# Kernel tuning notes

Hardware: AMD Instinct MI355X
Metric: run time of the kernel (lower is better)

The kernel has to match this reference:

```python
import jax, jax.numpy as jnp
import numpy as np

DIM = 256
BUFFER_SIZE = 64


def setup_inputs() -> dict:
    key = jax.random.key(0)
    k1, k2, k3 = jax.random.split(key, 3)
    B, S, D = 4, 4096, DIM
    d2 = 2 * D
    states = jax.random.normal(k1, (B, S, D, 2), dtype=jnp.float32)
    # nn.Linear weights, applied as x @ W.T (torch convention)
    W_q = jax.random.normal(k2, (d2, d2), dtype=jnp.float32) / np.sqrt(d2)
    W_k = jax.random.normal(k3, (d2, d2), dtype=jnp.float32) / np.sqrt(d2)
    return {"states": states, "W_q": W_q, "W_k": W_k}


def reference(states, W_q, W_k):
    B, S, D, _ = states.shape
    d2 = 2 * D
    states_flat = states.reshape(B, S, d2)                      # [B,S,2D]
    queries = jnp.einsum('bsd,ed->bse', states_flat, W_q)       # x @ W.T
    keys = jnp.einsum('bsd,ed->bse', states_flat, W_k)
    scale = d2 ** -0.5
    scores = jnp.einsum('bqe,bke->bqk', queries, keys) * scale  # [B,S,S]
    pos = jnp.arange(S)
    diff = pos[:, None] - pos[None, :]                          # i - j
    # causal (strictly past) AND within sliding window of buffer_size
    valid = (diff >= 1) & (diff <= BUFFER_SIZE)                 # [S,S]
    scores = jnp.where(valid[None, :, :], scores, -jnp.inf)
    attn = jax.nn.softmax(scores, axis=-1)
    attn = jnp.nan_to_num(attn, nan=0.0)                        # row 0 is all -inf -> 0
    retrieved = jnp.einsum('bqk,bkd->bqd', attn, states_flat)   # values = raw states
    return retrieved.reshape(B, S, D, 2), attn
```

## Files before the change

kernel.cpp:

```cpp
#include <hip/hip_runtime.h>
#include <hip/hip_bf16.h>
#include <cstdint>

typedef uint16_t u16;
typedef __attribute__((ext_vector_type(8))) short short8;
typedef __attribute__((ext_vector_type(4))) float f32x4;
typedef __attribute__((ext_vector_type(2))) float f32x2;
typedef __attribute__((ext_vector_type(4))) float fv4;

static constexpr int S = 4096;
static constexpr int D2 = 512;
static constexpr size_t RET_ELEMS = 16384ull * 512ull;
static constexpr float SCALE = 0.04419417382415922f;

__device__ __forceinline__ u16 f2bf(float f) {
  uint32_t u = __float_as_uint(f);
  u += 0x7fffu + ((u >> 16) & 1u);
  return (u16)(u >> 16);
}

__device__ __forceinline__ float bflo(uint32_t u) { return __uint_as_float(u << 16); }
__device__ __forceinline__ float bfhi(uint32_t u) { return __uint_as_float(u & 0xffff0000u); }

__global__ void cast_f32_bf16(const float* __restrict__ src, u16* __restrict__ dst, int n4) {
  int idx = blockIdx.x * blockDim.x + threadIdx.x;
  if (idx < n4) {
    float4 v = *(const float4*)(src + (size_t)idx * 4);
    ushort4 o;
    o.x = f2bf(v.x); o.y = f2bf(v.y); o.z = f2bf(v.z); o.w = f2bf(v.w);
    *(ushort4*)(dst + (size_t)idx * 4) = o;
  }
}

#define BM 128
#define BN 128
#define BK 32
#define LDSP 40

__global__ __launch_bounds__(256) void qk_gemm(
    const u16* __restrict__ Xb, const u16* __restrict__ Wqb, const u16* __restrict__ Wkb,
    u16* __restrict__ Qb, u16* __restrict__ Kb) {
  __shared__ u16 Xs[BM * LDSP];
  __shared__ u16 Ws[BN * LDSP];
  const int m0 = blockIdx.x * BM;
  const int sel = blockIdx.y >> 2;
  const int n0 = (blockIdx.y & 3) * BN;
  const u16* __restrict__ Wb = sel ? Wkb : Wqb;
  u16* __restrict__ Cb = sel ? Kb : Qb;

  const int t = threadIdx.x;
  const int lane = t & 63, w = t >> 6;
  const int wm = w >> 1, wn = w & 1;
  const int r16 = lane & 15, kg = lane >> 4;
  const int srow = t >> 2, skcol = (t & 3) * 8;

  f32x4 acc[4][4] = {};

  for (int kt = 0; kt < D2; kt += BK) {
    __syncthreads();
    for (int p = 0; p < 2; ++p) {
      int row = srow + p * 64;
      uint4 va = *(const uint4*)(Xb + (size_t)(m0 + row) * D2 + kt + skcol);
      *(uint4*)(Xs + row * LDSP + skcol) = va;
      uint4 vb = *(const uint4*)(Wb + (size_t)(n0 + row) * D2 + kt + skcol);
      *(uint4*)(Ws + row * LDSP + skcol) = vb;
    }
    __syncthreads();
    short8 a[4], b[4];
    for (int f = 0; f < 4; ++f) {
      a[f] = *(const short8*)(Xs + (wm * 64 + f * 16 + r16) * LDSP + kg * 8);
      b[f] = *(const short8*)(Ws + (wn * 64 + f * 16 + r16) * LDSP + kg * 8);
    }
    for (int fm = 0; fm < 4; ++fm)
      for (int fn = 0; fn < 4; ++fn)
        acc[fm][fn] = __builtin_amdgcn_mfma_f32_16x16x32_bf16(a[fm], b[fn], acc[fm][fn], 0, 0, 0);
  }

  for (int fm = 0; fm < 4; ++fm) {
    int grow = m0 + wm * 64 + fm * 16 + kg * 4;
    for (int fn = 0; fn < 4; ++fn) {
      int gcol = n0 + wn * 64 + fn * 16 + r16;
      for (int r = 0; r < 4; ++r)
        Cb[(size_t)(grow + r) * D2 + gcol] = f2bf(acc[fm][fn][r]);
    }
  }
}

__global__ __launch_bounds__(256, 4) void attn_kernel(
    const u16* __restrict__ Qb, const u16* __restrict__ Kb, const u16* __restrict__ Xb,
    float* __restrict__ out) {
  __shared__ float p_jm[4][80][16];

  const int bid = blockIdx.x;
  const int swz = (bid & 7) * 128 + (bid >> 3);
  const int w = threadIdx.x >> 6;
  const int lane = threadIdx.x & 63;
  const int qg = swz * 16;
  const int b = qg >> 12;
  const int i0 = qg & (S - 1);
  const int c15 = lane & 15;
  const int g = lane >> 4;

  const u16* kbat = Kb + (((size_t)b) << 12) * D2;
  const u16* qptr = Qb + (size_t)(qg + c15) * D2 + g * 8;
  const u16* kptr = kbat + (ptrdiff_t)(i0 - 64 + c15) * D2 + g * 8;
  float* azero = out + RET_ELEMS + (size_t)qg * S;

  f32x4 sc[5] = {};
  const fv4 z4 = {0.f, 0.f, 0.f, 0.f};
  #pragma unroll 1
  for (int s = 0; s < 16; ++s) {
    short8 qf = *(const short8*)(qptr + s * 32);
    #pragma unroll
    for (int r_ = 0; r_ < 4; ++r_) {
      const int rw = 4 * w + r_;
      const int i = i0 + rw;
      const int f = s * 64 + lane;
      const int flo = (i >= 64) ? ((i - 64) >> 2) : 0;
      const bool band = (i >= 1) && (f >= flo) && (f <= ((i - 1) >> 2));
      if (!band)
        __builtin_nontemporal_store(z4, (fv4*)(azero + (size_t)rw * S + 4 * f));
    }
    #pragma unroll
    for (int t = 0; t < 5; ++t) {
      short8 kf = *(const short8*)(kptr + t * (16 * D2) + s * 32);
      sc[t] = __builtin_amdgcn_mfma_f32_16x16x32_bf16(qf, kf, sc[t], 0, 0, 0);
    }
  }

  float sv[5][4];
  #pragma unroll
  for (int t = 0; t < 5; ++t)
    #pragma unroll
    for (int r = 0; r < 4; ++r) {
      const int m = 4 * g + r;
      const int rel = 16 * t + c15 - m;
      const int j = i0 - 64 + 16 * t + c15;
      const bool ok = (rel >= 0) && (rel < 64) && (j >= 0);
      sv[t][r] = ok ? sc[t][r] * SCALE : -INFINITY;
    }

  float p[5][4];
  #pragma unroll
  for (int r = 0; r < 4; ++r) {
    float mx = sv[0][r];
    #pragma unroll
    for (int t = 1; t < 5; ++t) mx = fmaxf(mx, sv[t][r]);
    #pragma unroll
    for (int off = 8; off; off >>= 1) mx = fmaxf(mx, __shfl_xor(mx, off));
    float e[5], sum = 0.f;
    #pragma unroll
    for (int t = 0; t < 5; ++t) {
      e[t] = (sv[t][r] == -INFINITY) ? 0.f : __expf(sv[t][r] - mx);
      sum += e[t];
    }
    #pragma unroll
    for (int off = 8; off; off >>= 1) sum += __shfl_xor(sum, off);
    const float rinv = (sum > 0.f) ? 1.f / sum : 0.f;
    #pragma unroll
    for (int t = 0; t < 5; ++t) p[t][r] = e[t] * rinv;
  }

  #pragma unroll
  for (int t = 0; t < 5; ++t)
    #pragma unroll
    for (int r = 0; r < 4; ++r)
      p_jm[w][16 * t + c15][4 * g + r] = p[t][r];

  {
    const int m2 = 4 * w + g;
    const int i = i0 + m2;
    if (i >= 1) {
      const int lo = (i >= 64) ? (i - 64) : 0;
      const int f0 = lo >> 2, f1 = (i - 1) >> 2;
      float* arow = azero + (size_t)m2 * S;
      #pragma unroll
      for (int pass = 0; pass < 2; ++pass) {
        const int f = f0 + c15 + 16 * pass;
        if (f <= f1) {
          fv4 v;
          #pragma unroll
          for (int c = 0; c < 4; ++c) {
            const int col = 4 * f + c;
            const bool in = (col >= lo) && (col <= i - 1);
            v[c] = in ? p_jm[w][col - i0 + 64][m2] : 0.f;
          }
          __builtin_nontemporal_store(v, (fv4*)(arow + 4 * f));
        }
      }
    }
  }

  f32x2 acc[16];
  #pragma unroll
  for (int m = 0; m < 16; ++m) acc[m] = (f32x2){0.f, 0.f};

  const int jstart = (i0 >= 64) ? 0 : (64 - i0);
  const u16* xcol = Xb + (((size_t)b) << 12) * D2 + (ptrdiff_t)(i0 - 64) * D2
                    + w * 128 + lane * 2;
  #pragma unroll 2
  for (int j = jstart; j < 79; ++j) {
    const uint32_t xu = *(const uint32_t*)(xcol + (size_t)j * D2);
    const f32x2 xv = {bflo(xu), bfhi(xu)};
    float pall[16];
    *(float4*)&pall[0]  = *(const float4*)&p_jm[w][j][0];
    *(float4*)&pall[4]  = *(const float4*)&p_jm[w][j][4];
    *(float4*)&pall[8]  = *(const float4*)&p_jm[w][j][8];
    *(float4*)&pall[12] = *(const float4*)&p_jm[w][j][12];
    #pragma unroll
    for (int m = 0; m < 16; ++m)
      acc[m] += (f32x2){pall[m], pall[m]} * xv;
  }

  #pragma unroll
  for (int m = 0; m < 16; ++m) {
    float* rr = out + (size_t)(qg + m) * D2 + w * 128 + lane * 2;
    __builtin_nontemporal_store(acc[m], (f32x2*)rr);
  }
}

extern "C" void kernel_launch(void* const* d_in, const int* in_sizes, int n_in,
                              void* d_out, int out_size, void* d_ws, size_t ws_size,
                              hipStream_t stream) {
  const float* states = (const float*)d_in[0];
  const float* W_q    = (const float*)d_in[1];
  const float* W_k    = (const float*)d_in[2];
  float* out = (float*)d_out;

  char* ws = (char*)d_ws;
  u16* Xb  = (u16*)(ws);
  u16* Qb  = (u16*)(ws + 16777216);
  u16* Kb  = (u16*)(ws + 33554432);
  u16* Wqb = (u16*)(ws + 50331648);
  u16* Wkb = (u16*)(ws + 50855936);

  cast_f32_bf16<<<8192, 256, 0, stream>>>(states, Xb, 2097152);
  cast_f32_bf16<<<256, 256, 0, stream>>>(W_q, Wqb, 65536);
  cast_f32_bf16<<<256, 256, 0, stream>>>(W_k, Wkb, 65536);

  qk_gemm<<<dim3(128, 8), 256, 0, stream>>>(Xb, Wqb, Wkb, Qb, Kb);

  attn_kernel<<<1024, 256, 0, stream>>>(Qb, Kb, Xb, out);
}
```

Baseline: 128.3 us.

## Fold Wq^T Wk into one matrix and compute scores against states in LDS

New measurement: 145.6 us. 13.5% more time.

```diff
diff --git a/kernel.cpp b/kernel.cpp
--- a/kernel.cpp
+++ b/kernel.cpp
@@ -5,7 +5,6 @@
 typedef uint16_t u16;
 typedef __attribute__((ext_vector_type(8))) short short8;
 typedef __attribute__((ext_vector_type(4))) float f32x4;
-typedef __attribute__((ext_vector_type(2))) float f32x2;
 typedef __attribute__((ext_vector_type(4))) float fv4;
 
 static constexpr int S = 4096;
@@ -32,21 +31,46 @@
   }
 }
 
+__global__ __launch_bounds__(256) void m_gemm(const float* __restrict__ Wq,
+                                              const float* __restrict__ Wk,
+                                              u16* __restrict__ MbT) {
+  __shared__ float aq[8][32], ak[8][32];
+  const int d0 = (blockIdx.x & 15) * 32;
+  const int e0 = (blockIdx.x >> 4) * 32;
+  const int tx = threadIdx.x & 15, ty = threadIdx.x >> 4;
+  float acc[2][2] = {};
+  for (int k0 = 0; k0 < 512; k0 += 8) {
+    __syncthreads();
+    const int r = threadIdx.x >> 5, c = threadIdx.x & 31;
+    aq[r][c] = Wq[(size_t)(k0 + r) * 512 + d0 + c];
+    ak[r][c] = Wk[(size_t)(k0 + r) * 512 + e0 + c];
+    __syncthreads();
+    #pragma unroll
+    for (int kk = 0; kk < 8; ++kk) {
+      const float q0 = aq[kk][2 * ty], q1 = aq[kk][2 * ty + 1];
+      const float w0 = ak[kk][2 * tx], w1 = ak[kk][2 * tx + 1];
+      acc[0][0] += q0 * w0; acc[0][1] += q0 * w1;
+      acc[1][0] += q1 * w0; acc[1][1] += q1 * w1;
+    }
+  }
+  #pragma unroll
+  for (int a = 0; a < 2; ++a)
+    #pragma unroll
+    for (int c = 0; c < 2; ++c)
+      MbT[(size_t)(e0 + 2 * tx + c) * 512 + d0 + 2 * ty + a] = f2bf(acc[a][c] * SCALE);
+}
+
 #define BM 128
 #define BN 128
 #define BK 32
 #define LDSP 40
 
-__global__ __launch_bounds__(256) void qk_gemm(
-    const u16* __restrict__ Xb, const u16* __restrict__ Wqb, const u16* __restrict__ Wkb,
-    u16* __restrict__ Qb, u16* __restrict__ Kb) {
+__global__ __launch_bounds__(256) void q_gemm(
+    const u16* __restrict__ Xb, const u16* __restrict__ Bt, u16* __restrict__ Qp) {
   __shared__ u16 Xs[BM * LDSP];
   __shared__ u16 Ws[BN * LDSP];
   const int m0 = blockIdx.x * BM;
-  const int sel = blockIdx.y >> 2;
-  const int n0 = (blockIdx.y & 3) * BN;
-  const u16* __restrict__ Wb = sel ? Wkb : Wqb;
-  u16* __restrict__ Cb = sel ? Kb : Qb;
+  const int n0 = blockIdx.y * BN;
 
   const int t = threadIdx.x;
   const int lane = t & 63, w = t >> 6;
@@ -62,7 +86,7 @@
       int row = srow + p * 64;
       uint4 va = *(const uint4*)(Xb + (size_t)(m0 + row) * D2 + kt + skcol);
       *(uint4*)(Xs + row * LDSP + skcol) = va;
-      uint4 vb = *(const uint4*)(Wb + (size_t)(n0 + row) * D2 + kt + skcol);
+      uint4 vb = *(const uint4*)(Bt + (size_t)(n0 + row) * D2 + kt + skcol);
       *(uint4*)(Ws + row * LDSP + skcol) = vb;
     }
     __syncthreads();
@@ -81,109 +105,138 @@
     for (int fn = 0; fn < 4; ++fn) {
       int gcol = n0 + wn * 64 + fn * 16 + r16;
       for (int r = 0; r < 4; ++r)
-        Cb[(size_t)(grow + r) * D2 + gcol] = f2bf(acc[fm][fn][r]);
-    }
-  }
-}
-
-__global__ __launch_bounds__(256, 4) void attn_kernel(
-    const u16* __restrict__ Qb, const u16* __restrict__ Kb, const u16* __restrict__ Xb,
-    float* __restrict__ out) {
+        Qp[(size_t)(grow + r) * D2 + gcol] = f2bf(acc[fm][fn][r]);
+    }
+  }
+}
+
+__global__ __launch_bounds__(512) void attn_kernel(
+    const u16* __restrict__ Qp, const u16* __restrict__ Xb, float* __restrict__ out) {
+  __shared__ u16 xs[128 * 512];
   __shared__ float p_jm[4][80][16];
 
   const int bid = blockIdx.x;
-  const int swz = (bid & 7) * 128 + (bid >> 3);
+  const int swz = (bid & 7) * 32 + (bid >> 3);
   const int w = threadIdx.x >> 6;
   const int lane = threadIdx.x & 63;
-  const int qg = swz * 16;
+  const int qg = swz * 64;
   const int b = qg >> 12;
   const int i0 = qg & (S - 1);
-  const int c15 = lane & 15;
-  const int g = lane >> 4;
-
-  const u16* kbat = Kb + (((size_t)b) << 12) * D2;
-  const u16* qptr = Qb + (size_t)(qg + c15) * D2 + g * 8;
-  const u16* kptr = kbat + (ptrdiff_t)(i0 - 64 + c15) * D2 + g * 8;
-  float* azero = out + RET_ELEMS + (size_t)qg * S;
-
-  f32x4 sc[5] = {};
+  const int c15 = lane & 15, g = lane >> 4;
+  const int grp = w & 3, dh = w >> 2;
+  const int i0g = i0 + grp * 16;
+  const int qgg = qg + grp * 16;
+
+  float* aout = out + RET_ELEMS + (size_t)qg * S;
   const fv4 z4 = {0.f, 0.f, 0.f, 0.f};
-  #pragma unroll 1
-  for (int s = 0; s < 16; ++s) {
-    short8 qf = *(const short8*)(qptr + s * 32);
-    #pragma unroll
-    for (int r_ = 0; r_ < 4; ++r_) {
-      const int rw = 4 * w + r_;
-      const int i = i0 + rw;
-      const int f = s * 64 + lane;
+
+  {
+    const u16* xbat = Xb + (((size_t)b) << 12) * D2;
+    const int tid = threadIdx.x;
+    #pragma unroll
+    for (int cch = 0; cch < 16; ++cch) {
+      const int idx8 = tid + (cch << 9);
+      const int rl = idx8 >> 6;
+      const int cb = (idx8 & 63) << 4;
+      int gr = i0 - 64 + rl; gr = gr < 0 ? 0 : gr;
+      const uint4 v = *(const uint4*)(xbat + (size_t)gr * D2 + (cb >> 1));
+      *(uint4*)((char*)xs + rl * 1024 + (cb ^ ((rl & 7) << 4))) = v;
+    }
+  }
+  __syncthreads();
+
+  if (dh == 0) {
+    const u16* qptr = Qp + (size_t)(qgg + c15) * D2 + g * 8;
+    f32x4 sc[5] = {};
+    #pragma unroll 1
+    for (int s = 0; s < 16; ++s) {
+      const short8 qf = *(const short8*)(qptr + s * 32);
+      #pragma unroll
+      for (int t = 0; t < 5; ++t) {
+        const int rl = grp * 16 + 16 * t + c15;
+        const int cb = ((s << 6) + (g << 4)) ^ ((rl & 7) << 4);
+        const short8 kf = *(const short8*)((const char*)xs + rl * 1024 + cb);
+        sc[t] = __builtin_amdgcn_mfma_f32_16x16x32_bf16(qf, kf, sc[t], 0, 0, 0);
+      }
+    }
+
+    float sv[5][4];
+    #pragma unroll
+    for (int t = 0; t < 5; ++t)
+      #pragma unroll
+      for (int r = 0; r < 4; ++r) {
+        const int m = 4 * g + r;
+        const int rel = 16 * t + c15 - m;
+        const int j = i0g - 64 + 16 * t + c15;
+        const bool ok = (rel >= 0) && (rel < 64) && (j >= 0);
+        sv[t][r] = ok ? sc[t][r] : -INFINITY;
+      }
+
+    float p[5][4];
+    #pragma unroll
+    for (int r = 0; r < 4; ++r) {
+      float mx = sv[0][r];
+      #pragma unroll
+      for (int t = 1; t < 5; ++t) mx = fmaxf(mx, sv[t][r]);
+      #pragma unroll
+      for (int off = 8; off; off >>= 1) mx = fmaxf(mx, __shfl_xor(mx, off));
+      float e[5], sum = 0.f;
+      #pragma unroll
+      for (int t = 0; t < 5; ++t) {
+        e[t] = (sv[t][r] == -INFINITY) ? 0.f : __expf(sv[t][r] - mx);
+        sum += e[t];
+      }
+      #pragma unroll
+      for (int off = 8; off; off >>= 1) sum += __shfl_xor(sum, off);
+      const float rinv = (sum > 0.f) ? 1.f / sum : 0.f;
+      #pragma unroll
+      for (int t = 0; t < 5; ++t) p[t][r] = e[t] * rinv;
+    }
+
+    #pragma unroll
+    for (int t = 0; t < 5; ++t)
+      #pragma unroll
+      for (int r = 0; r < 4; ++r)
+        p_jm[grp][16 * t + c15][4 * g + r] = p[t][r];
+  } else {
+    #pragma unroll 1
+    for (int rr = 0; rr < 16; ++rr) {
+      const int m2 = grp * 16 + rr;
+      const int i = i0 + m2;
       const int flo = (i >= 64) ? ((i - 64) >> 2) : 0;
-      const bool band = (i >= 1) && (f >= flo) && (f <= ((i - 1) >> 2));
-      if (!band)
-        __builtin_nontemporal_store(z4, (fv4*)(azero + (size_t)rw * S + 4 * f));
-    }
-    #pragma unroll
-    for (int t = 0; t < 5; ++t) {
-      short8 kf = *(const short8*)(kptr + t * (16 * D2) + s * 32);
-      sc[t] = __builtin_amdgcn_mfma_f32_16x16x32_bf16(qf, kf, sc[t], 0, 0, 0);
-    }
-  }
-
-  float sv[5][4];
-  #pragma unroll
-  for (int t = 0; t < 5; ++t)
-    #pragma unroll
-    for (int r = 0; r < 4; ++r) {
-      const int m = 4 * g + r;
-      const int rel = 16 * t + c15 - m;
-      const int j = i0 - 64 + 16 * t + c15;
-      const bool ok = (rel >= 0) && (rel < 64) && (j >= 0);
-      sv[t][r] = ok ? sc[t][r] * SCALE : -INFINITY;
-    }
-
-  float p[5][4];
-  #pragma unroll
-  for (int r = 0; r < 4; ++r) {
-    float mx = sv[0][r];
-    #pragma unroll
-    for (int t = 1; t < 5; ++t) mx = fmaxf(mx, sv[t][r]);
-    #pragma unroll
-    for (int off = 8; off; off >>= 1) mx = fmaxf(mx, __shfl_xor(mx, off));
-    float e[5], sum = 0.f;
-    #pragma unroll
-    for (int t = 0; t < 5; ++t) {
-      e[t] = (sv[t][r] == -INFINITY) ? 0.f : __expf(sv[t][r] - mx);
-      sum += e[t];
-    }
-    #pragma unroll
-    for (int off = 8; off; off >>= 1) sum += __shfl_xor(sum, off);
-    const float rinv = (sum > 0.f) ? 1.f / sum : 0.f;
-    #pragma unroll
-    for (int t = 0; t < 5; ++t) p[t][r] = e[t] * rinv;
-  }
-
-  #pragma unroll
-  for (int t = 0; t < 5; ++t)
-    #pragma unroll
-    for (int r = 0; r < 4; ++r)
-      p_jm[w][16 * t + c15][4 * g + r] = p[t][r];
+      const int f1b = (i - 1) >> 2;
+      float* arow = aout + (size_t)m2 * S;
+      #pragma unroll 4
+      for (int s = 0; s < 16; ++s) {
+        const int f = s * 64 + lane;
+        const bool band = (i >= 1) && (f >= flo) && (f <= f1b);
+        if (!band) __builtin_nontemporal_store(z4, (fv4*)(arow + 4 * f));
+      }
+    }
+  }
+  __syncthreads();
 
   {
-    const int m2 = 4 * w + g;
+    const int mm = dh * 8 + g * 2 + (c15 >> 3);
+    const int m2 = grp * 16 + mm;
     const int i = i0 + m2;
+    const int c8 = c15 & 7;
     if (i >= 1) {
       const int lo = (i >= 64) ? (i - 64) : 0;
       const int f0 = lo >> 2, f1 = (i - 1) >> 2;
-      float* arow = azero + (size_t)m2 * S;
-      #pragma unroll
-      for (int pass = 0; pass < 2; ++pass) {
-        const int f = f0 + c15 + 16 * pass;
+      float* arow = aout + (size_t)m2 * S;
+      #pragma unroll
+      for (int pass = 0; pass < 3; ++pass) {
+        const int f = f0 + c8 + (pass << 3);
         if (f <= f1) {
           fv4 v;
           #pragma unroll
           for (int c = 0; c < 4; ++c) {
             const int col = 4 * f + c;
-            const bool in = (col >= lo) && (col <= i - 1);
-            v[c] = in ? p_jm[w][col - i0 + 64][m2] : 0.f;
+            const bool in = (col >= lo) && (col < i);
+            int rel = col - (i0g - 64);
+            rel = rel < 0 ? 0 : rel;
+            v[c] = in ? p_jm[grp][rel][mm] : 0.f;
           }
           __builtin_nontemporal_store(v, (fv4*)(arow + 4 * f));
         }
@@ -191,31 +244,34 @@
     }
   }
 
-  f32x2 acc[16];
-  #pragma unroll
-  for (int m = 0; m < 16; ++m) acc[m] = (f32x2){0.f, 0.f};
-
-  const int jstart = (i0 >= 64) ? 0 : (64 - i0);
-  const u16* xcol = Xb + (((size_t)b) << 12) * D2 + (ptrdiff_t)(i0 - 64) * D2
-                    + w * 128 + lane * 2;
+  f32x4 acc[16] = {};
+  const int jstart = (i0g >= 64) ? 0 : (64 - i0g);
+  const int cbase = (dh << 9) + (lane << 3);
   #pragma unroll 2
   for (int j = jstart; j < 79; ++j) {
-    const uint32_t xu = *(const uint32_t*)(xcol + (size_t)j * D2);
-    const f32x2 xv = {bflo(xu), bfhi(xu)};
-    float pall[16];
-    *(float4*)&pall[0]  = *(const float4*)&p_jm[w][j][0];
-    *(float4*)&pall[4]  = *(const float4*)&p_jm[w][j][4];
-    *(float4*)&pall[8]  = *(const float4*)&p_jm[w][j][8];
-    *(float4*)&pall[12] = *(const float4*)&p_jm[w][j][12];
-    #pragma unroll
-    for (int m = 0; m < 16; ++m)
-      acc[m] += (f32x2){pall[m], pall[m]} * xv;
-  }
-
-  #pragma unroll
+    const int rl = grp * 16 + j;
+    const int cb = cbase ^ ((rl & 7) << 4);
+    const uint2 xu = *(const uint2*)((const char*)xs + rl * 1024 + cb);
+    const float x0 = bflo(xu.x), x1 = bfhi(xu.x);
+    const float x2 = bflo(xu.y), x3 = bfhi(xu.y);
+    alignas(16) float pall[16];
+    *(float4*)&pall[0]  = *(const float4*)&p_jm[grp][j][0];
+    *(float4*)&pall[4]  = *(const float4*)&p_jm[grp][j][4];
+    *(float4*)&pall[8]  = *(const float4*)&p_jm[grp][j][8];
+    *(float4*)&pall[12] = *(const float4*)&p_jm[grp][j][12];
+    #pragma unroll
+    for (int m = 0; m < 16; ++m) {
+      const fv4 xv = {x0, x1, x2, x3};
+      const fv4 pp = {pall[m], pall[m], pall[m], pall[m]};
+      acc[m] += pp * xv;
+    }
+  }
+
+  #pragma unroll 1
   for (int m = 0; m < 16; ++m) {
-    float* rr = out + (size_t)(qg + m) * D2 + w * 128 + lane * 2;
-    __builtin_nontemporal_store(acc[m], (f32x2*)rr);
+    float* rr = out + (size_t)(qgg + m) * D2 + (dh << 8) + lane * 4;
+    const fv4 r = {acc[m][0], acc[m][1], acc[m][2], acc[m][3]};
+    __builtin_nontemporal_store(r, (fv4*)rr);
   }
 }
 
@@ -229,16 +285,11 @@
 
   char* ws = (char*)d_ws;
   u16* Xb  = (u16*)(ws);
-  u16* Qb  = (u16*)(ws + 16777216);
-  u16* Kb  = (u16*)(ws + 33554432);
-  u16* Wqb = (u16*)(ws + 50331648);
-  u16* Wkb = (u16*)(ws + 50855936);
+  u16* Qp  = (u16*)(ws + 16777216);
+  u16* MbT = (u16*)(ws + 33554432);
 
   cast_f32_bf16<<<8192, 256, 0, stream>>>(states, Xb, 2097152);
-  cast_f32_bf16<<<256, 256, 0, stream>>>(W_q, Wqb, 65536);
-  cast_f32_bf16<<<256, 256, 0, stream>>>(W_k, Wkb, 65536);
-
-  qk_gemm<<<dim3(128, 8), 256, 0, stream>>>(Xb, Wqb, Wkb, Qb, Kb);
-
-  attn_kernel<<<1024, 256, 0, stream>>>(Qb, Kb, Xb, out);
-}
+  m_gemm<<<256, 256, 0, stream>>>(W_q, W_k, MbT);
+  q_gemm<<<dim3(128, 4), 256, 0, stream>>>(Xb, MbT, Qp);
+  attn_kernel<<<256, 512, 0, stream>>>(Qp, Xb, out);
+}
```

## Fold Wq^T·Wk into one matrix and replace the separate K projection

Applied to the files above, without the earlier changes.

Result: slower. 184.1 us (+43.4%).

```diff
diff --git a/kernel.cpp b/kernel.cpp
--- a/kernel.cpp
+++ b/kernel.cpp
@@ -32,21 +32,46 @@
   }
 }
 
+__global__ __launch_bounds__(256) void m_gemm(const float* __restrict__ Wq,
+                                              const float* __restrict__ Wk,
+                                              u16* __restrict__ MbT) {
+  __shared__ float aq[8][32], ak[8][32];
+  const int d0 = (blockIdx.x & 15) * 32;
+  const int e0 = (blockIdx.x >> 4) * 32;
+  const int tx = threadIdx.x & 15, ty = threadIdx.x >> 4;
+  float acc[2][2] = {};
+  for (int k0 = 0; k0 < 512; k0 += 8) {
+    __syncthreads();
+    const int r = threadIdx.x >> 5, c = threadIdx.x & 31;
+    aq[r][c] = Wq[(size_t)(k0 + r) * 512 + d0 + c];
+    ak[r][c] = Wk[(size_t)(k0 + r) * 512 + e0 + c];
+    __syncthreads();
+    #pragma unroll
+    for (int kk = 0; kk < 8; ++kk) {
+      const float q0 = aq[kk][2 * ty], q1 = aq[kk][2 * ty + 1];
+      const float w0 = ak[kk][2 * tx], w1 = ak[kk][2 * tx + 1];
+      acc[0][0] += q0 * w0; acc[0][1] += q0 * w1;
+      acc[1][0] += q1 * w0; acc[1][1] += q1 * w1;
+    }
+  }
+  #pragma unroll
+  for (int a = 0; a < 2; ++a)
+    #pragma unroll
+    for (int c = 0; c < 2; ++c)
+      MbT[(size_t)(e0 + 2 * tx + c) * 512 + d0 + 2 * ty + a] = f2bf(acc[a][c] * SCALE);
+}
+
 #define BM 128
 #define BN 128
 #define BK 32
 #define LDSP 40
 
-__global__ __launch_bounds__(256) void qk_gemm(
-    const u16* __restrict__ Xb, const u16* __restrict__ Wqb, const u16* __restrict__ Wkb,
-    u16* __restrict__ Qb, u16* __restrict__ Kb) {
+__global__ __launch_bounds__(256) void q_gemm(
+    const u16* __restrict__ Xb, const u16* __restrict__ Bt, u16* __restrict__ Qp) {
   __shared__ u16 Xs[BM * LDSP];
   __shared__ u16 Ws[BN * LDSP];
   const int m0 = blockIdx.x * BM;
-  const int sel = blockIdx.y >> 2;
-  const int n0 = (blockIdx.y & 3) * BN;
-  const u16* __restrict__ Wb = sel ? Wkb : Wqb;
-  u16* __restrict__ Cb = sel ? Kb : Qb;
+  const int n0 = blockIdx.y * BN;
 
   const int t = threadIdx.x;
   const int lane = t & 63, w = t >> 6;
@@ -62,7 +87,7 @@
       int row = srow + p * 64;
       uint4 va = *(const uint4*)(Xb + (size_t)(m0 + row) * D2 + kt + skcol);
       *(uint4*)(Xs + row * LDSP + skcol) = va;
-      uint4 vb = *(const uint4*)(Wb + (size_t)(n0 + row) * D2 + kt + skcol);
+      uint4 vb = *(const uint4*)(Bt + (size_t)(n0 + row) * D2 + kt + skcol);
       *(uint4*)(Ws + row * LDSP + skcol) = vb;
     }
     __syncthreads();
@@ -81,14 +106,13 @@
     for (int fn = 0; fn < 4; ++fn) {
       int gcol = n0 + wn * 64 + fn * 16 + r16;
       for (int r = 0; r < 4; ++r)
-        Cb[(size_t)(grow + r) * D2 + gcol] = f2bf(acc[fm][fn][r]);
+        Qp[(size_t)(grow + r) * D2 + gcol] = f2bf(acc[fm][fn][r]);
     }
   }
 }
 
 __global__ __launch_bounds__(256, 4) void attn_kernel(
-    const u16* __restrict__ Qb, const u16* __restrict__ Kb, const u16* __restrict__ Xb,
-    float* __restrict__ out) {
+    const u16* __restrict__ Qp, const u16* __restrict__ Xb, float* __restrict__ out) {
   __shared__ float p_jm[4][80][16];
 
   const int bid = blockIdx.x;
@@ -98,32 +122,19 @@
   const int qg = swz * 16;
   const int b = qg >> 12;
   const int i0 = qg & (S - 1);
-  const int c15 = lane & 15;
-  const int g = lane >> 4;
-
-  const u16* kbat = Kb + (((size_t)b) << 12) * D2;
-  const u16* qptr = Qb + (size_t)(qg + c15) * D2 + g * 8;
-  const u16* kptr = kbat + (ptrdiff_t)(i0 - 64 + c15) * D2 + g * 8;
-  float* azero = out + RET_ELEMS + (size_t)qg * S;
+  const int c15 = lane & 15, g = lane >> 4;
+
+  const u16* xbat = Xb + (((size_t)b) << 12) * D2;
+  const u16* qptr = Qp + (size_t)(qg + c15) * D2 + g * 8;
+  const u16* kptr = xbat + (ptrdiff_t)(i0 - 64 + c15) * D2 + g * 8;
 
   f32x4 sc[5] = {};
-  const fv4 z4 = {0.f, 0.f, 0.f, 0.f};
   #pragma unroll 1
   for (int s = 0; s < 16; ++s) {
-    short8 qf = *(const short8*)(qptr + s * 32);
-    #pragma unroll
-    for (int r_ = 0; r_ < 4; ++r_) {
-      const int rw = 4 * w + r_;
-      const int i = i0 + rw;
-      const int f = s * 64 + lane;
-      const int flo = (i >= 64) ? ((i - 64) >> 2) : 0;
-      const bool band = (i >= 1) && (f >= flo) && (f <= ((i - 1) >> 2));
-      if (!band)
-        __builtin_nontemporal_store(z4, (fv4*)(azero + (size_t)rw * S + 4 * f));
-    }
+    const short8 qf = *(const short8*)(qptr + s * 32);
     #pragma unroll
     for (int t = 0; t < 5; ++t) {
-      short8 kf = *(const short8*)(kptr + t * (16 * D2) + s * 32);
+      const short8 kf = *(const short8*)(kptr + t * (16 * D2) + s * 32);
       sc[t] = __builtin_amdgcn_mfma_f32_16x16x32_bf16(qf, kf, sc[t], 0, 0, 0);
     }
   }
@@ -137,7 +148,7 @@
       const int rel = 16 * t + c15 - m;
       const int j = i0 - 64 + 16 * t + c15;
       const bool ok = (rel >= 0) && (rel < 64) && (j >= 0);
-      sv[t][r] = ok ? sc[t][r] * SCALE : -INFINITY;
+      sv[t][r] = ok ? sc[t][r] : -INFINITY;
     }
 
   float p[5][4];
@@ -173,7 +184,7 @@
     if (i >= 1) {
       const int lo = (i >= 64) ? (i - 64) : 0;
       const int f0 = lo >> 2, f1 = (i - 1) >> 2;
-      float* arow = azero + (size_t)m2 * S;
+      float* arow = out + RET_ELEMS + (size_t)(qg + m2) * S;
       #pragma unroll
       for (int pass = 0; pass < 2; ++pass) {
         const int f = f0 + c15 + 16 * pass;
@@ -182,8 +193,10 @@
           #pragma unroll
           for (int c = 0; c < 4; ++c) {
             const int col = 4 * f + c;
-            const bool in = (col >= lo) && (col <= i - 1);
-            v[c] = in ? p_jm[w][col - i0 + 64][m2] : 0.f;
+            const bool in = (col >= lo) && (col < i);
+            int rel = col - i0 + 64;
+            rel = (rel < 0) ? 0 : (rel > 79 ? 79 : rel);
+            v[c] = in ? p_jm[w][rel][m2] : 0.f;
           }
           __builtin_nontemporal_store(v, (fv4*)(arow + 4 * f));
         }
@@ -196,13 +209,12 @@
   for (int m = 0; m < 16; ++m) acc[m] = (f32x2){0.f, 0.f};
 
   const int jstart = (i0 >= 64) ? 0 : (64 - i0);
-  const u16* xcol = Xb + (((size_t)b) << 12) * D2 + (ptrdiff_t)(i0 - 64) * D2
-                    + w * 128 + lane * 2;
+  const u16* xcol = xbat + (ptrdiff_t)(i0 - 64) * D2 + w * 128 + lane * 2;
   #pragma unroll 2
   for (int j = jstart; j < 79; ++j) {
     const uint32_t xu = *(const uint32_t*)(xcol + (size_t)j * D2);
     const f32x2 xv = {bflo(xu), bfhi(xu)};
-    float pall[16];
+    alignas(16) float pall[16];
     *(float4*)&pall[0]  = *(const float4*)&p_jm[w][j][0];
     *(float4*)&pall[4]  = *(const float4*)&p_jm[w][j][4];
     *(float4*)&pall[8]  = *(const float4*)&p_jm[w][j][8];
@@ -228,17 +240,14 @@
   float* out = (float*)d_out;
 
   char* ws = (char*)d_ws;
-  u16* Xb  = (u16*)(ws);
-  u16* Qb  = (u16*)(ws + 16777216);
-  u16* Kb  = (u16*)(ws + 33554432);
-  u16* Wqb = (u16*)(ws + 50331648);
-  u16* Wkb = (u16*)(ws + 50855936);
+  u16* Qp  = (u16*)(ws);
+  u16* Xb  = (u16*)(ws + 16777216);
+  u16* MbT = (u16*)(ws + 33554432);
+
+  hipMemsetAsync(out + RET_ELEMS, 0, 16384ull * 4096ull * 4ull, stream);
 
   cast_f32_bf16<<<8192, 256, 0, stream>>>(states, Xb, 2097152);
-  cast_f32_bf16<<<256, 256, 0, stream>>>(W_q, Wqb, 65536);
-  cast_f32_bf16<<<256, 256, 0, stream>>>(W_k, Wkb, 65536);
-
-  qk_gemm<<<dim3(128, 8), 256, 0, stream>>>(Xb, Wqb, Wkb, Qb, Kb);
-
-  attn_kernel<<<1024, 256, 0, stream>>>(Qb, Kb, Xb, out);
-}
+  m_gemm<<<256, 256, 0, stream>>>(W_q, W_k, MbT);
+  q_gemm<<<dim3(128, 4), 256, 0, stream>>>(Xb, MbT, Qp);
+  attn_kernel<<<1024, 256, 0, stream>>>(Qp, Xb, out);
+}
```
